# Kernel tuning notes

Hardware: AMD Instinct MI355X
Metric: run time of the kernel (lower is better)

The kernel has to match this reference:

```python
import jax, jax.numpy as jnp
import numpy as np

EPS_BN = 1e-5
EPS_NORM = 1e-12
NUM_HEADS = 8


def _bn_relu(x):
    # BatchNorm2d in training mode with fresh params (gamma=1, beta=0), then ReLU.
    m = x.mean((0, 2, 3), keepdims=True)
    v = x.var((0, 2, 3), keepdims=True)  # biased variance, as PyTorch uses for normalization
    return jax.nn.relu((x - m) * jax.lax.rsqrt(v + EPS_BN))


def _conv3(x, w, groups=1):
    # 3x3 conv, stride 1, padding 1 (NCHW / OIHW)
    return jax.lax.conv_general_dilated(
        x, w, (1, 1), ((1, 1), (1, 1)),
        dimension_numbers=('NCHW', 'OIHW', 'NCHW'),
        feature_group_count=groups)


def _encoder(x, w1, w2, w3):
    # Conv1x1 -> BN -> ReLU -> Conv k2 s2 -> BN -> ReLU -> Conv1x1 -> BN -> ReLU
    x = _bn_relu(jnp.einsum('bihw,oi->bohw', x, w1))
    b, c, h, w = x.shape
    # k=2,s=2 conv as a reshape + einsum (non-overlapping 2x2 patches)
    x = _bn_relu(jnp.einsum('bchpwq,ocpq->bohw', x.reshape(b, c, h // 2, 2, w // 2, 2), w2))
    return _bn_relu(jnp.einsum('bihw,oi->bohw', x, w3))


def _decoder(x, w1, w2, w3):
    # ConvT1x1 -> BN -> ReLU -> ConvT k2 s2 -> BN -> ReLU -> ConvT1x1 -> BN -> ReLU
    x = _bn_relu(jnp.einsum('bihw,io->bohw', x, w1))
    # ConvTranspose k=2,s=2: each input pixel expands to a 2x2 block
    y = jnp.einsum('bihw,iopq->bohpwq', x, w2)
    b, o, h, p, w, q = y.shape
    x = _bn_relu(y.reshape(b, o, h * p, w * q))
    return _bn_relu(jnp.einsum('bihw,io->bohw', x, w3))


def _l2norm(x):
    # F.normalize(dim=-1) with eps=1e-12
    return x / jnp.maximum(jnp.linalg.norm(x, axis=-1, keepdims=True), EPS_NORM)


def setup_inputs() -> dict:
    key = jax.random.key(0)
    ks = jax.random.split(key, 13)
    B, C, H, W = 8, 256, 64, 64
    d = C // 4  # attention dim after self.divide

    def rn(k, shape, s=0.1):
        return jax.random.normal(k, shape, jnp.float32) * s

    return {
        'x': jax.random.normal(ks[0], (B, C, H, W), jnp.float32),
        'y': jax.random.normal(ks[1], (B, C, H, W), jnp.float32),
        'temperature': jnp.ones((NUM_HEADS, 1, 1), jnp.float32),
        'enc_w1': rn(ks[2], (d // 2, C)),
        'enc_w2': rn(ks[3], (d // 2, d // 2, 2, 2)),
        'enc_w3': rn(ks[4], (d, d // 2)),
        'kv_w': rn(ks[5], (2 * d, d)),
        'kv_dw_w': rn(ks[6], (2 * d, 1, 3, 3)),
        'q_w': rn(ks[7], (d, d)),
        'q_dw_w': rn(ks[8], (d, d, 3, 3)),
        'proj_w': rn(ks[9], (d, d)),
        'dec_w1': rn(ks[10], (d, 2 * d)),
        'dec_w2': rn(ks[11], (2 * d, 2 * d, 2, 2)),
        'dec_w3': rn(ks[12], (2 * d, 4 * d)),
    }


def reference(x, y, temperature, enc_w1, enc_w2, enc_w3, kv_w, kv_dw_w,
              q_w, q_dw_w, proj_w, dec_w1, dec_w2, dec_w3):
    # Shared freshly-built encoder applied to both x and y (same weights,
    # BN batch stats computed per call).
    x = _encoder(x, enc_w1, enc_w2, enc_w3)
    y = _encoder(y, enc_w1, enc_w2, enc_w3)
    b, c, h, w = x.shape  # c = 64, h = w = 32

    kv = _conv3(jnp.einsum('bihw,oi->bohw', x, kv_w), kv_dw_w, groups=2 * c)
    k, v = jnp.split(kv, 2, axis=1)
    q = _conv3(jnp.einsum('bihw,oi->bohw', y, q_w), q_dw_w)  # regular 3x3 conv

    ch = c // NUM_HEADS
    heads = lambda t: t.reshape(b, NUM_HEADS, ch, h * w)  # b head c (h w)
    q, k, v = heads(q), heads(k), heads(v)
    q = _l2norm(q)
    k = _l2norm(k)
    temp = temperature[None]  # [1, head, 1, 1]

    # Spatial attention: [b, head, hw, hw]
    attn_s = jax.nn.softmax(jnp.einsum('bhcn,bhcm->bhnm', q, k) * temp, axis=-1)
    out_s = jnp.einsum('bhcn,bhnm->bhcm', v, attn_s).reshape(b, c, h, w)
    out_s = jnp.einsum('bihw,oi->bohw', out_s, proj_w)

    # Channel attention: [b, head, c, c]
    attn_c = jax.nn.softmax(jnp.einsum('bhcn,bhdn->bhcd', q, k) * temp, axis=-1)
    out_c = jnp.einsum('bhcd,bhdn->bhcn', attn_c, v).reshape(b, c, h, w)
    out_c = jnp.einsum('bihw,oi->bohw', out_c, proj_w)

    return _decoder(out_s + out_c, dec_w1, dec_w2, dec_w3)
```

## Files before the change

### kernel.cpp

```cpp
#include <hip/hip_runtime.h>
#include <hip/hip_bf16.h>

#define EPS_BN 1e-5f

template<int OT, bool HASBN, bool HASSTATS>
__global__ __launch_bounds__(256) void conv1x1_kernel(
    const float* __restrict__ in0, const float* __restrict__ in1,
    const float* __restrict__ w, float* __restrict__ out,
    const float* __restrict__ stIn, float* __restrict__ stOut,
    int I, int O, int P, int wio, int zsplit, float invN)
{
  __shared__ float wl[2048];
  __shared__ float bnm[256], bnr[256];
  int tid = threadIdx.x;
  int o0 = blockIdx.y*OT;
  int z  = blockIdx.z;
  int t  = (z >= zsplit) ? 1 : 0;
  int b  = t ? (z - zsplit) : z;
  const float* in = t ? in1 : in0;

  for(int idx=tid; idx<I*OT; idx+=256){
    int i = idx/OT, j = idx - i*OT;
    wl[idx] = wio ? w[(size_t)i*O + o0 + j] : w[(size_t)(o0+j)*I + i];
  }
  if(HASBN){
    for(int i=tid; i<I; i+=256){
      float s  = stIn[((size_t)t*I + i)*2];
      float s2 = stIn[((size_t)t*I + i)*2+1];
      float m  = s*invN;
      bnm[i] = m;
      bnr[i] = rsqrtf(s2*invN - m*m + EPS_BN);
    }
  }
  __syncthreads();

  int p4 = blockIdx.x*256 + tid;
  const float4* inb = (const float4*)(in + (size_t)b*I*P) + p4;
  int P4 = P >> 2;

  float acc[OT][4];
#pragma unroll
  for(int j=0;j<OT;j++){ acc[j][0]=acc[j][1]=acc[j][2]=acc[j][3]=0.f; }

  float4 vb[8];
  for(int i0=0;i0<I;i0+=8){
#pragma unroll
    for(int u=0;u<8;u++) vb[u] = inb[(size_t)(i0+u)*P4];
#pragma unroll
    for(int u=0;u<8;u++){
      float4 v = vb[u];
      if(HASBN){
        float m = bnm[i0+u], r = bnr[i0+u];
        v.x = fmaxf((v.x-m)*r, 0.f); v.y = fmaxf((v.y-m)*r, 0.f);
        v.z = fmaxf((v.z-m)*r, 0.f); v.w = fmaxf((v.w-m)*r, 0.f);
      }
      const float* wr = &wl[(i0+u)*OT];
#pragma unroll
      for(int j=0;j<OT;j++){
        float wv = wr[j];
        acc[j][0] = fmaf(wv, v.x, acc[j][0]);
        acc[j][1] = fmaf(wv, v.y, acc[j][1]);
        acc[j][2] = fmaf(wv, v.z, acc[j][2]);
        acc[j][3] = fmaf(wv, v.w, acc[j][3]);
      }
    }
  }

  float4* ob = (float4*)(out + ((size_t)z*O + o0)*P) + p4;
#pragma unroll
  for(int j=0;j<OT;j++){
    float4 vv = {acc[j][0], acc[j][1], acc[j][2], acc[j][3]};
    ob[(size_t)j*P4] = vv;
  }

  if(HASSTATS){
#pragma unroll
    for(int j=0;j<OT;j++){
      float s  = acc[j][0]+acc[j][1]+acc[j][2]+acc[j][3];
      float s2 = acc[j][0]*acc[j][0]+acc[j][1]*acc[j][1]
               + acc[j][2]*acc[j][2]+acc[j][3]*acc[j][3];
      for(int off=32; off>0; off>>=1){
        s  += __shfl_down(s,  off, 64);
        s2 += __shfl_down(s2, off, 64);
      }
      if((tid & 63)==0){
        atomicAdd(&stOut[((size_t)t*O + o0 + j)*2],   s);
        atomicAdd(&stOut[((size_t)t*O + o0 + j)*2+1], s2);
      }
    }
  }
}

__global__ __launch_bounds__(256) void conv2x2s2_bn_kernel(
    const float* __restrict__ in, const float* __restrict__ w,
    float* __restrict__ out, const float* __restrict__ stIn,
    float* __restrict__ stOut, float invN)
{
  __shared__ float wl[512];
  __shared__ float bnm[32], bnr[32];
  int tid = threadIdx.x;
  int o0 = blockIdx.x*4;
  int z  = blockIdx.y;
  int t  = (z >= 8) ? 1 : 0;

  for(int idx=tid; idx<512; idx+=256){
    int pq = idx & 3, r = idx >> 2;
    int i = r >> 2, j = r & 3;
    wl[idx] = w[(((size_t)(o0+j)*32 + i)*4) + pq];
  }
  if(tid < 32){
    float s  = stIn[((size_t)t*32 + tid)*2];
    float s2 = stIn[((size_t)t*32 + tid)*2+1];
    float m  = s*invN;
    bnm[tid] = m;
    bnr[tid] = rsqrtf(s2*invN - m*m + EPS_BN);
  }
  __syncthreads();

  int h  = tid >> 3;
  int wg = tid & 7;
  int cb = wg*8;

  float acc[4][4];
#pragma unroll
  for(int j=0;j<4;j++) for(int k=0;k<4;k++) acc[j][k]=0.f;

  float4 pre[8];
  for(int i0=0;i0<32;i0+=4){
#pragma unroll
    for(int u=0;u<4;u++){
      pre[2*u]   = *(const float4*)(in + (((size_t)z*32+i0+u)*64 + 2*h)*64 + cb);
      pre[2*u+1] = *(const float4*)(in + (((size_t)z*32+i0+u)*64 + 2*h)*64 + cb + 4);
    }
#pragma unroll
    for(int u=0;u<4;u++){
      int i = i0+u;
      const float4* r1p = (const float4*)(in + (((size_t)z*32+i)*64 + 2*h+1)*64 + cb);
      float4 a0 = pre[2*u], a1 = pre[2*u+1];
      float4 b0 = r1p[0], b1 = r1p[1];
      float m = bnm[i], r = bnr[i];
      float t0[8] = {a0.x,a0.y,a0.z,a0.w,a1.x,a1.y,a1.z,a1.w};
      float t1[8] = {b0.x,b0.y,b0.z,b0.w,b1.x,b1.y,b1.z,b1.w};
#pragma unroll
      for(int e=0;e<8;e++){
        t0[e] = fmaxf((t0[e]-m)*r, 0.f);
        t1[e] = fmaxf((t1[e]-m)*r, 0.f);
      }
#pragma unroll
      for(int j=0;j<4;j++){
        const float* wj = &wl[(i*4+j)*4];
#pragma unroll
        for(int k=0;k<4;k++){
          acc[j][k] = fmaf(wj[0], t0[2*k],   acc[j][k]);
          acc[j][k] = fmaf(wj[1], t0[2*k+1], acc[j][k]);
          acc[j][k] = fmaf(wj[2], t1[2*k],   acc[j][k]);
          acc[j][k] = fmaf(wj[3], t1[2*k+1], acc[j][k]);
        }
      }
    }
  }

#pragma unroll
  for(int j=0;j<4;j++){
    float4 vv = {acc[j][0],acc[j][1],acc[j][2],acc[j][3]};
    *(float4*)(out + ((size_t)z*32 + o0+j)*1024 + h*32 + wg*4) = vv;
  }
#pragma unroll
  for(int j=0;j<4;j++){
    float s  = acc[j][0]+acc[j][1]+acc[j][2]+acc[j][3];
    float s2 = acc[j][0]*acc[j][0]+acc[j][1]*acc[j][1]
             + acc[j][2]*acc[j][2]+acc[j][3]*acc[j][3];
    for(int off=32; off>0; off>>=1){
      s  += __shfl_down(s,  off, 64);
      s2 += __shfl_down(s2, off, 64);
    }
    if((tid & 63)==0){
      atomicAdd(&stOut[((size_t)t*32 + o0 + j)*2],   s);
      atomicAdd(&stOut[((size_t)t*32 + o0 + j)*2+1], s2);
    }
  }
}

__global__ __launch_bounds__(256) void upsample2x2_bn_kernel(
    const float* __restrict__ in, const float* __restrict__ w,
    float* __restrict__ out, const float* __restrict__ stIn,
    float* __restrict__ stOut, float invN)
{
  __shared__ float wl[1024];
  __shared__ float bnm[128], bnr[128];
  int tid = threadIdx.x;
  int o0 = blockIdx.x*2;
  int b  = blockIdx.y;

  for(int idx=tid; idx<1024; idx+=256){
    int pq = idx & 3, r = idx >> 2;
    int i = r >> 1, j = r & 1;
    wl[idx] = w[((size_t)i*128 + o0+j)*4 + pq];
  }
  if(tid < 128){
    float s  = stIn[(size_t)tid*2];
    float s2 = stIn[(size_t)tid*2+1];
    float m  = s*invN;
    bnm[tid] = m;
    bnr[tid] = rsqrtf(s2*invN - m*m + EPS_BN);
  }
  __syncthreads();

  int h  = tid >> 3;
  int wg = tid & 7;
  int w0 = wg*4;

  float acc[2][16];
#pragma unroll
  for(int j=0;j<2;j++) for(int e=0;e<16;e++) acc[j][e]=0.f;

  float4 vb4[8];
  for(int i0=0;i0<128;i0+=8){
#pragma unroll
    for(int u=0;u<8;u++)
      vb4[u] = *(const float4*)(in + (((size_t)b*128+i0+u)*1024) + h*32 + w0);
#pragma unroll
    for(int u=0;u<8;u++){
      int i = i0+u;
      float4 v = vb4[u];
      float m = bnm[i], r = bnr[i];
      float vk[4] = {fmaxf((v.x-m)*r,0.f), fmaxf((v.y-m)*r,0.f),
                     fmaxf((v.z-m)*r,0.f), fmaxf((v.w-m)*r,0.f)};
#pragma unroll
      for(int j=0;j<2;j++){
        const float* wj = &wl[(i*2+j)*4];
#pragma unroll
        for(int pq=0;pq<4;pq++){
#pragma unroll
          for(int k=0;k<4;k++)
            acc[j][pq*4+k] = fmaf(wj[pq], vk[k], acc[j][pq*4+k]);
        }
      }
    }
  }

#pragma unroll
  for(int j=0;j<2;j++){
    float* ob = out + ((size_t)b*128 + o0+j)*4096;
#pragma unroll
    for(int p=0;p<2;p++){
      float4 A = {acc[j][(p*2+0)*4+0], acc[j][(p*2+1)*4+0],
                  acc[j][(p*2+0)*4+1], acc[j][(p*2+1)*4+1]};
      float4 B = {acc[j][(p*2+0)*4+2], acc[j][(p*2+1)*4+2],
                  acc[j][(p*2+0)*4+3], acc[j][(p*2+1)*4+3]};
      *(float4*)(ob + (2*h+p)*64 + 2*w0)     = A;
      *(float4*)(ob + (2*h+p)*64 + 2*w0 + 4) = B;
    }
  }

#pragma unroll
  for(int j=0;j<2;j++){
    float s=0.f, s2=0.f;
#pragma unroll
    for(int e=0;e<16;e++){ s += acc[j][e]; s2 += acc[j][e]*acc[j][e]; }
    for(int off=32; off>0; off>>=1){
      s  += __shfl_down(s,  off, 64);
      s2 += __shfl_down(s2, off, 64);
    }
    if((tid & 63)==0){
      atomicAdd(&stOut[((size_t)(o0+j))*2],   s);
      atomicAdd(&stOut[((size_t)(o0+j))*2+1], s2);
    }
  }
}

__global__ __launch_bounds__(256) void bn_final_kernel(
    float* __restrict__ x, const float* __restrict__ st, float invN)
{
  int idx4 = blockIdx.x*256 + threadIdx.x;
  int c = (idx4 >> 10) & 255;
  float s  = st[(size_t)c*2];
  float s2 = st[(size_t)c*2+1];
  float m  = s*invN;
  float r  = rsqrtf(s2*invN - m*m + EPS_BN);
  float4 v = ((float4*)x)[idx4];
  v.x = fmaxf((v.x-m)*r, 0.f); v.y = fmaxf((v.y-m)*r, 0.f);
  v.z = fmaxf((v.z-m)*r, 0.f); v.w = fmaxf((v.w-m)*r, 0.f);
  ((float4*)x)[idx4] = v;
}

__global__ __launch_bounds__(256) void dwconv3x3_kernel(
    const float* __restrict__ in, const float* __restrict__ w,
    float* __restrict__ out, int C, int H, int Wd)
{
  int idx = blockIdx.x*256 + threadIdx.x;
  int c = blockIdx.y, b = blockIdx.z;
  if(idx >= H*Wd) return;
  int h = idx / Wd, x = idx - h*Wd;
  const float* inp = in + ((size_t)b*C + c)*H*Wd;
  float acc = 0.f;
#pragma unroll
  for(int p=0;p<3;p++){
    int hh = h + p - 1;
    if((unsigned)hh >= (unsigned)H) continue;
#pragma unroll
    for(int q=0;q<3;q++){
      int wv = x + q - 1;
      if((unsigned)wv >= (unsigned)Wd) continue;
      acc += w[c*9 + p*3 + q] * inp[hh*Wd + wv];
    }
  }
  out[((size_t)b*C + c)*H*Wd + idx] = acc;
}

__global__ __launch_bounds__(256) void conv3x3_kernel(
    const float* __restrict__ in, const float* __restrict__ w,
    float* __restrict__ out, int IC, int H, int Wd)
{
  int o = blockIdx.y, b = blockIdx.z;
  __shared__ float wl[576];
  for(int t=threadIdx.x; t<IC*9; t+=256) wl[t] = w[(size_t)o*IC*9 + t];
  __syncthreads();
  int idx = blockIdx.x*256 + threadIdx.x;
  if(idx >= H*Wd) return;
  int h = idx / Wd, x = idx - h*Wd;
  const float* inb = in + (size_t)b*IC*H*Wd;
  float acc = 0.f;
  for(int i=0;i<IC;i++){
    const float* inp = inb + (size_t)i*H*Wd;
    const float* wp  = wl + i*9;
#pragma unroll
    for(int p=0;p<3;p++){
      int hh = h + p - 1;
      if((unsigned)hh >= (unsigned)H) continue;
      const float* row = inp + hh*Wd;
#pragma unroll
      for(int q=0;q<3;q++){
        int wv = x + q - 1;
        if((unsigned)wv >= (unsigned)Wd) continue;
        acc = fmaf(wp[p*3+q], row[wv], acc);
      }
    }
  }
  out[((size_t)b*gridDim.y + o)*H*Wd + idx] = acc;
}

__global__ __launch_bounds__(256) void l2norm_kernel(
    float* __restrict__ q, float* __restrict__ kv)
{
  int r = blockIdx.x;
  float* p;
  if(r < 512){ int b=r>>6, c=r&63; p = q + ((size_t)b*64+c)*1024; }
  else { int rr=r-512; int b=rr>>6, c=rr&63; p = kv + ((size_t)b*128+c)*1024; }
  int tid = threadIdx.x;
  float4 v = ((float4*)p)[tid];
  float s = v.x*v.x + v.y*v.y + v.z*v.z + v.w*v.w;
  __shared__ float ls[256];
  ls[tid]=s; __syncthreads();
  for(int st=128; st>0; st>>=1){ if(tid<st) ls[tid]+=ls[tid+st]; __syncthreads(); }
  float scale = 1.f / fmaxf(sqrtf(ls[0]), 1e-12f);
  v.x*=scale; v.y*=scale; v.z*=scale; v.w*=scale;
  ((float4*)p)[tid] = v;
}

__global__ __launch_bounds__(256) void attn_pass1(
    const float* __restrict__ q, const float* __restrict__ kv,
    const float* __restrict__ temp, float* __restrict__ iden_out)
{
  int chunk = blockIdx.x, hh = blockIdx.y, b = blockIdx.z;
  int tid = threadIdx.x;
  __shared__ __align__(16) float kl[8192];
  const float* kb = kv + ((size_t)b*128 + hh*8)*1024;
  for(int t=tid;t<8192;t+=256){ int c=t>>10, m=t&1023; kl[m*8+c]=kb[t]; }
  __syncthreads();
  int n = chunk*256 + tid;
  const float* qp = q + ((size_t)b*64 + hh*8)*1024 + n;
  float qr[8];
#pragma unroll
  for(int c=0;c<8;c++) qr[c]=qp[(size_t)c*1024];
  float th = temp[hh];
  float mxb = fabsf(th);
  const float4* kl4 = (const float4*)kl;
  float den = 0.f;
  for(int m=0;m<1024;m++){
    float4 a = kl4[2*m], a2 = kl4[2*m+1];
    float s = qr[0]*a.x+qr[1]*a.y+qr[2]*a.z+qr[3]*a.w
            + qr[4]*a2.x+qr[5]*a2.y+qr[6]*a2.z+qr[7]*a2.w;
    den += __expf(s*th - mxb);
  }
  int bh = b*8+hh;
  iden_out[(size_t)bh*1024+n] = 1.f/den;
}

__global__ __launch_bounds__(256) void attn_pass2(
    const float* __restrict__ q, const float* __restrict__ kv,
    const float* __restrict__ temp, const float* __restrict__ iden_in,
    float* __restrict__ out)
{
  int chunk = blockIdx.x, hh = blockIdx.y, b = blockIdx.z;
  int tid = threadIdx.x;
  __shared__ __align__(16) float ql[4096];
  __shared__ __align__(16) float vl[4096];
  const float* qb = q  + ((size_t)b*64 + hh*8)*1024;
  const float* vb = kv + ((size_t)b*128 + 64 + hh*8)*1024;
  int bh = b*8+hh;
  int m = chunk*256 + tid;
  const float* kb = kv + ((size_t)b*128 + hh*8)*1024 + m;
  float kr[8];
#pragma unroll
  for(int c=0;c<8;c++) kr[c]=kb[(size_t)c*1024];
  float th = temp[hh];
  float mxb = fabsf(th);
  const float* idp = iden_in + (size_t)bh*1024;
  float acc[8] = {0,0,0,0,0,0,0,0};
  for(int half=0; half<2; half++){
    int n0 = half*512;
    __syncthreads();
    for(int t=tid; t<4096; t+=256){
      int c = t>>9, n = t&511;
      ql[n*8+c] = qb[(size_t)c*1024 + n0 + n];
      vl[n*8+c] = vb[(size_t)c*1024 + n0 + n];
    }
    __syncthreads();
    const float4* ql4 = (const float4*)ql;
    const float4* vl4 = (const float4*)vl;
    for(int n=0;n<512;n++){
      float4 qa = ql4[2*n], qa2 = ql4[2*n+1];
      float s = kr[0]*qa.x+kr[1]*qa.y+kr[2]*qa.z+kr[3]*qa.w
              + kr[4]*qa2.x+kr[5]*qa2.y+kr[6]*qa2.z+kr[7]*qa2.w;
      float pp = __expf(s*th - mxb) * idp[n0+n];
      float4 va = vl4[2*n], va2 = vl4[2*n+1];
      acc[0]+=pp*va.x; acc[1]+=pp*va.y; acc[2]+=pp*va.z; acc[3]+=pp*va.w;
      acc[4]+=pp*va2.x; acc[5]+=pp*va2.y; acc[6]+=pp*va2.z; acc[7]+=pp*va2.w;
    }
  }
  float* ob = out + ((size_t)b*64 + hh*8)*1024 + m;
#pragma unroll
  for(int c=0;c<8;c++) ob[(size_t)c*1024] = acc[c];
}

__global__ __launch_bounds__(256) void attn_channel(
    const float* __restrict__ q, const float* __restrict__ kv,
    const float* __restrict__ temp, float* out)
{
  int hh = blockIdx.x, b = blockIdx.y;
  __shared__ float kl[8192];
  const float* qb = q  + ((size_t)b*64 + hh*8)*1024;
  const float* kb = kv + ((size_t)b*128 + hh*8)*1024;
  const float* vb = kv + ((size_t)b*128 + 64 + hh*8)*1024;
  int tid = threadIdx.x;
  for(int t=tid;t<8192;t+=256) kl[t]=kb[t];
  __syncthreads();
  __shared__ float part[256];
  __shared__ float a[64];
  {
    int pair = tid >> 2, seg = tid & 3;
    int c = pair >> 3, d = pair & 7;
    const float* qrow = qb + (size_t)c*1024 + seg*256;
    const float* krow = kl + d*1024 + seg*256;
    float s = 0.f;
#pragma unroll 4
    for(int n=0;n<256;n++) s += qrow[n]*krow[n];
    part[tid] = s;
  }
  __syncthreads();
  if(tid < 64){
    float g = part[tid*4]+part[tid*4+1]+part[tid*4+2]+part[tid*4+3];
    part[tid] = g * temp[hh];
  }
  __syncthreads();
  if(tid < 8){
    float mx = -3.4e38f;
    for(int d=0;d<8;d++) mx = fmaxf(mx, part[tid*8+d]);
    float den = 0.f;
    float e[8];
    for(int d=0;d<8;d++){ e[d] = __expf(part[tid*8+d]-mx); den+=e[d]; }
    float inv = 1.f/den;
    for(int d=0;d<8;d++) a[tid*8+d] = e[d]*inv;
  }
  __syncthreads();
  float* ob = out + ((size_t)b*64 + hh*8)*1024;
  for(int n=tid;n<1024;n+=256){
    float vv[8];
#pragma unroll
    for(int d=0;d<8;d++) vv[d] = vb[(size_t)d*1024+n];
#pragma unroll
    for(int c=0;c<8;c++){
      float s = 0.f;
#pragma unroll
      for(int d=0;d<8;d++) s += a[c*8+d]*vv[d];
      ob[(size_t)c*1024+n] += s;
    }
  }
}

extern "C" void kernel_launch(void* const* d_in, const int* in_sizes, int n_in,
                              void* d_out, int out_size, void* d_ws, size_t ws_size,
                              hipStream_t stream)
{
  (void)in_sizes; (void)n_in; (void)out_size; (void)ws_size;
  const float* x      = (const float*)d_in[0];
  const float* y      = (const float*)d_in[1];
  const float* temp   = (const float*)d_in[2];
  const float* enc_w1 = (const float*)d_in[3];
  const float* enc_w2 = (const float*)d_in[4];
  const float* enc_w3 = (const float*)d_in[5];
  const float* kv_w   = (const float*)d_in[6];
  const float* kv_dw_w= (const float*)d_in[7];
  const float* q_w    = (const float*)d_in[8];
  const float* q_dw_w = (const float*)d_in[9];
  const float* proj_w = (const float*)d_in[10];
  const float* dec_w1 = (const float*)d_in[11];
  const float* dec_w2 = (const float*)d_in[12];
  const float* dec_w3 = (const float*)d_in[13];
  float* out = (float*)d_out;

  float* W   = (float*)d_ws;
  float* ST  = W;
  float* ST0 = ST;
  float* ST1 = ST + 128;
  float* ST2 = ST + 256;
  float* ST3 = ST + 512;
  float* ST4 = ST + 768;
  float* ST5 = ST + 1024;
  float* A    = W + 2048;
  float* E1   = A;
  float* KV1  = A;
  float* QPre = A + 1048576;
  float* ATTN = A;
  float* PROJ = A + 524288;
  float* D1   = A + 1048576;
  float* E2   = W + 2099200;
  float* E3   = W + 2623488;
  float* KV   = W + 3672064;
  float* Q    = W + 4720640;
  float* IDEN = W + 5244928;
  float* D2   = W + 2099200;

  const float inv32k = 1.f/32768.f, inv8k = 1.f/8192.f;

  hipMemsetAsync(ST, 0, 2048*sizeof(float), stream);

  conv1x1_kernel<4,false,true><<<dim3(4,8,16),256,0,stream>>>(
      x, y, enc_w1, E1, nullptr, ST0, 256, 32, 4096, 0, 8, 0.f);
  conv2x2s2_bn_kernel<<<dim3(8,16),256,0,stream>>>(E1, enc_w2, E2, ST0, ST1, inv32k);
  conv1x1_kernel<2,true,true><<<dim3(1,32,16),256,0,stream>>>(
      E2, E2 + (size_t)8*32*1024, enc_w3, E3, ST1, ST2, 32, 64, 1024, 0, 8, inv8k);

  conv1x1_kernel<4,true,false><<<dim3(1,32,8),256,0,stream>>>(
      E3, E3, kv_w, KV1, ST2, nullptr, 64, 128, 1024, 0, 999, inv8k);
  dwconv3x3_kernel<<<dim3(4,128,8),256,0,stream>>>(KV1, kv_dw_w, KV, 128, 32, 32);
  conv1x1_kernel<2,true,false><<<dim3(1,32,8),256,0,stream>>>(
      E3 + (size_t)8*64*1024, E3, q_w, QPre, ST2 + 128, nullptr, 64, 64, 1024, 0, 999, inv8k);
  conv3x3_kernel<<<dim3(4,64,8),256,0,stream>>>(QPre, q_dw_w, Q, 64, 32, 32);

  l2norm_kernel<<<1024,256,0,stream>>>(Q, KV);

  attn_pass1<<<dim3(4,8,8),256,0,stream>>>(Q, KV, temp, IDEN);
  attn_pass2<<<dim3(4,8,8),256,0,stream>>>(Q, KV, temp, IDEN, ATTN);
  attn_channel<<<dim3(8,8),256,0,stream>>>(Q, KV, temp, ATTN);

  conv1x1_kernel<2,false,false><<<dim3(1,32,8),256,0,stream>>>(
      ATTN, ATTN, proj_w, PROJ, nullptr, nullptr, 64, 64, 1024, 0, 999, 0.f);

  conv1x1_kernel<4,false,true><<<dim3(1,32,8),256,0,stream>>>(
      PROJ, PROJ, dec_w1, D1, nullptr, ST3, 64, 128, 1024, 1, 999, 0.f);
  upsample2x2_bn_kernel<<<dim3(64,8),256,0,stream>>>(D1, dec_w2, D2, ST3, ST4, inv8k);
  conv1x1_kernel<8,true,true><<<dim3(4,32,8),256,0,stream>>>(
      D2, D2, dec_w3, out, ST4, ST5, 128, 256, 4096, 1, 999, inv32k);
  bn_final_kernel<<<8192,256,0,stream>>>(out, ST5, inv32k);
}
```

Baseline: 678.1 us.

## Split attention passes across key halves with atomics, add tiled encoder conv

Adds a register-tiled first encoder 1x1 conv kernel that computes 4x4 output blocks per thread from shared-memory tiles, with wave-shuffle stat reduction. Both spatial attention passes are split into two halves over the reduction dimension, doubling the block count. Partial results are combined through atomicAdd into buffers zeroed beforehand by memset. The passes also use padded shared-memory strides, pre-scale q and k by temperature, and unroll by two. Two 1x1 convs get smaller output tiles and more blocks, trading extra atomics and memsets for more parallelism on a small grid.

```diff
diff --git a/kernel.cpp b/kernel.cpp
--- a/kernel.cpp
+++ b/kernel.cpp
@@ -2,6 +2,78 @@
 #include <hip/hip_bf16.h>
 
 #define EPS_BN 1e-5f
+
+__global__ __launch_bounds__(256) void conv1x1_enc1_kernel(
+    const float* __restrict__ in0, const float* __restrict__ in1,
+    const float* __restrict__ w, float* __restrict__ out,
+    float* __restrict__ stOut)
+{
+  __shared__ float il[32*128];
+  __shared__ float wt[32*32];
+  int tid  = threadIdx.x;
+  int tile = blockIdx.x;
+  int z    = blockIdx.y;
+  int t    = z >> 3;
+  const float* in  = t ? in1 : in0;
+  const float* inb = in + ((size_t)(z&7))*256*4096 + tile*128;
+  int cg = tid & 31;
+  int og = tid >> 5;
+
+  float acc[4][4];
+#pragma unroll
+  for(int j=0;j<4;j++){ acc[j][0]=acc[j][1]=acc[j][2]=acc[j][3]=0.f; }
+
+  for(int k0=0; k0<256; k0+=32){
+    __syncthreads();
+#pragma unroll
+    for(int u=0;u<4;u++){
+      int fid = tid + u*256;
+      int ch = fid >> 5, c4 = fid & 31;
+      ((float4*)il)[fid] = *(const float4*)(inb + (size_t)(k0+ch)*4096 + c4*4);
+    }
+#pragma unroll
+    for(int u=0;u<4;u++){
+      int idx = tid + u*256;
+      int o = idx >> 5, ch = idx & 31;
+      wt[ch*32 + o] = w[(size_t)o*256 + k0 + ch];
+    }
+    __syncthreads();
+#pragma unroll 8
+    for(int ch=0; ch<32; ch++){
+      float4 v  = ((float4*)il)[ch*32 + cg];
+      float4 wv = ((float4*)wt)[ch*8 + og];
+      acc[0][0]=fmaf(wv.x,v.x,acc[0][0]); acc[0][1]=fmaf(wv.x,v.y,acc[0][1]);
+      acc[0][2]=fmaf(wv.x,v.z,acc[0][2]); acc[0][3]=fmaf(wv.x,v.w,acc[0][3]);
+      acc[1][0]=fmaf(wv.y,v.x,acc[1][0]); acc[1][1]=fmaf(wv.y,v.y,acc[1][1]);
+      acc[1][2]=fmaf(wv.y,v.z,acc[1][2]); acc[1][3]=fmaf(wv.y,v.w,acc[1][3]);
+      acc[2][0]=fmaf(wv.z,v.x,acc[2][0]); acc[2][1]=fmaf(wv.z,v.y,acc[2][1]);
+      acc[2][2]=fmaf(wv.z,v.z,acc[2][2]); acc[2][3]=fmaf(wv.z,v.w,acc[2][3]);
+      acc[3][0]=fmaf(wv.w,v.x,acc[3][0]); acc[3][1]=fmaf(wv.w,v.y,acc[3][1]);
+      acc[3][2]=fmaf(wv.w,v.z,acc[3][2]); acc[3][3]=fmaf(wv.w,v.w,acc[3][3]);
+    }
+  }
+
+  float* ob = out + ((size_t)z*32 + og*4)*4096 + tile*128 + cg*4;
+#pragma unroll
+  for(int j=0;j<4;j++){
+    float4 vv = {acc[j][0],acc[j][1],acc[j][2],acc[j][3]};
+    *(float4*)(ob + (size_t)j*4096) = vv;
+  }
+#pragma unroll
+  for(int j=0;j<4;j++){
+    float s  = acc[j][0]+acc[j][1]+acc[j][2]+acc[j][3];
+    float s2 = acc[j][0]*acc[j][0]+acc[j][1]*acc[j][1]
+             + acc[j][2]*acc[j][2]+acc[j][3]*acc[j][3];
+    for(int off=16; off>0; off>>=1){
+      s  += __shfl_down(s,  off, 64);
+      s2 += __shfl_down(s2, off, 64);
+    }
+    if((tid & 31)==0){
+      atomicAdd(&stOut[((size_t)t*32 + og*4 + j)*2],   s);
+      atomicAdd(&stOut[((size_t)t*32 + og*4 + j)*2+1], s2);
+    }
+  }
+}
 
 template<int OT, bool HASBN, bool HASSTATS>
 __global__ __launch_bounds__(256) void conv1x1_kernel(
@@ -360,78 +432,88 @@
 
 __global__ __launch_bounds__(256) void attn_pass1(
     const float* __restrict__ q, const float* __restrict__ kv,
-    const float* __restrict__ temp, float* __restrict__ iden_out)
-{
-  int chunk = blockIdx.x, hh = blockIdx.y, b = blockIdx.z;
+    const float* __restrict__ temp, float* __restrict__ den_out)
+{
+  int bx = blockIdx.x, hh = blockIdx.y, b = blockIdx.z;
+  int nchunk = bx >> 1, mh = bx & 1;
   int tid = threadIdx.x;
-  __shared__ __align__(16) float kl[8192];
-  const float* kb = kv + ((size_t)b*128 + hh*8)*1024;
-  for(int t=tid;t<8192;t+=256){ int c=t>>10, m=t&1023; kl[m*8+c]=kb[t]; }
-  __syncthreads();
-  int n = chunk*256 + tid;
+  __shared__ __align__(16) float kl[512*12];
+  const float* kb = kv + ((size_t)b*128 + hh*8)*1024 + mh*512;
+  for(int t=tid;t<4096;t+=256){ int c=t>>9, m=t&511; kl[m*12+c]=kb[(size_t)c*1024+m]; }
+  __syncthreads();
+  int n = nchunk*256 + tid;
   const float* qp = q + ((size_t)b*64 + hh*8)*1024 + n;
-  float qr[8];
-#pragma unroll
-  for(int c=0;c<8;c++) qr[c]=qp[(size_t)c*1024];
   float th = temp[hh];
   float mxb = fabsf(th);
+  float qr[8];
+#pragma unroll
+  for(int c=0;c<8;c++) qr[c]=qp[(size_t)c*1024]*th;
   const float4* kl4 = (const float4*)kl;
-  float den = 0.f;
-  for(int m=0;m<1024;m++){
-    float4 a = kl4[2*m], a2 = kl4[2*m+1];
-    float s = qr[0]*a.x+qr[1]*a.y+qr[2]*a.z+qr[3]*a.w
-            + qr[4]*a2.x+qr[5]*a2.y+qr[6]*a2.z+qr[7]*a2.w;
-    den += __expf(s*th - mxb);
-  }
-  int bh = b*8+hh;
-  iden_out[(size_t)bh*1024+n] = 1.f/den;
+  float den = 0.f, den2 = 0.f;
+  for(int m=0;m<512;m+=2){
+    float4 a  = kl4[m*3],     a2 = kl4[m*3+1];
+    float4 bt = kl4[(m+1)*3], b2 = kl4[(m+1)*3+1];
+    float s0 = qr[0]*a.x+qr[1]*a.y+qr[2]*a.z+qr[3]*a.w
+             + qr[4]*a2.x+qr[5]*a2.y+qr[6]*a2.z+qr[7]*a2.w;
+    float s1 = qr[0]*bt.x+qr[1]*bt.y+qr[2]*bt.z+qr[3]*bt.w
+             + qr[4]*b2.x+qr[5]*b2.y+qr[6]*b2.z+qr[7]*b2.w;
+    den  += __expf(s0 - mxb);
+    den2 += __expf(s1 - mxb);
+  }
+  atomicAdd(&den_out[((size_t)(b*8+hh))*1024+n], den+den2);
 }
 
 __global__ __launch_bounds__(256) void attn_pass2(
     const float* __restrict__ q, const float* __restrict__ kv,
-    const float* __restrict__ temp, const float* __restrict__ iden_in,
+    const float* __restrict__ temp, const float* __restrict__ den,
     float* __restrict__ out)
 {
-  int chunk = blockIdx.x, hh = blockIdx.y, b = blockIdx.z;
+  int bx = blockIdx.x, hh = blockIdx.y, b = blockIdx.z;
+  int mchunk = bx >> 1, nh = bx & 1;
   int tid = threadIdx.x;
-  __shared__ __align__(16) float ql[4096];
-  __shared__ __align__(16) float vl[4096];
-  const float* qb = q  + ((size_t)b*64 + hh*8)*1024;
-  const float* vb = kv + ((size_t)b*128 + 64 + hh*8)*1024;
+  __shared__ __align__(16) float ql[512*12];
+  __shared__ __align__(16) float vl[512*12];
+  __shared__ float idl[512];
   int bh = b*8+hh;
-  int m = chunk*256 + tid;
+  int n0 = nh*512;
+  const float* qb = q  + ((size_t)b*64 + hh*8)*1024 + n0;
+  const float* vb = kv + ((size_t)b*128 + 64 + hh*8)*1024 + n0;
+  for(int t=tid;t<4096;t+=256){
+    int c=t>>9, n=t&511;
+    ql[n*12+c] = qb[(size_t)c*1024+n];
+    vl[n*12+c] = vb[(size_t)c*1024+n];
+  }
+  for(int u=tid;u<512;u+=256) idl[u] = 1.f/den[(size_t)bh*1024 + n0 + u];
+  __syncthreads();
+  int m = mchunk*256 + tid;
   const float* kb = kv + ((size_t)b*128 + hh*8)*1024 + m;
-  float kr[8];
-#pragma unroll
-  for(int c=0;c<8;c++) kr[c]=kb[(size_t)c*1024];
   float th = temp[hh];
   float mxb = fabsf(th);
-  const float* idp = iden_in + (size_t)bh*1024;
+  float kr[8];
+#pragma unroll
+  for(int c=0;c<8;c++) kr[c]=kb[(size_t)c*1024]*th;
   float acc[8] = {0,0,0,0,0,0,0,0};
-  for(int half=0; half<2; half++){
-    int n0 = half*512;
-    __syncthreads();
-    for(int t=tid; t<4096; t+=256){
-      int c = t>>9, n = t&511;
-      ql[n*8+c] = qb[(size_t)c*1024 + n0 + n];
-      vl[n*8+c] = vb[(size_t)c*1024 + n0 + n];
-    }
-    __syncthreads();
-    const float4* ql4 = (const float4*)ql;
-    const float4* vl4 = (const float4*)vl;
-    for(int n=0;n<512;n++){
-      float4 qa = ql4[2*n], qa2 = ql4[2*n+1];
-      float s = kr[0]*qa.x+kr[1]*qa.y+kr[2]*qa.z+kr[3]*qa.w
-              + kr[4]*qa2.x+kr[5]*qa2.y+kr[6]*qa2.z+kr[7]*qa2.w;
-      float pp = __expf(s*th - mxb) * idp[n0+n];
-      float4 va = vl4[2*n], va2 = vl4[2*n+1];
-      acc[0]+=pp*va.x; acc[1]+=pp*va.y; acc[2]+=pp*va.z; acc[3]+=pp*va.w;
-      acc[4]+=pp*va2.x; acc[5]+=pp*va2.y; acc[6]+=pp*va2.z; acc[7]+=pp*va2.w;
-    }
+  const float4* ql4 = (const float4*)ql;
+  const float4* vl4 = (const float4*)vl;
+  for(int n=0;n<512;n+=2){
+    float4 qa = ql4[n*3],     qa2 = ql4[n*3+1];
+    float4 qb4= ql4[(n+1)*3], qb2 = ql4[(n+1)*3+1];
+    float s0 = kr[0]*qa.x+kr[1]*qa.y+kr[2]*qa.z+kr[3]*qa.w
+             + kr[4]*qa2.x+kr[5]*qa2.y+kr[6]*qa2.z+kr[7]*qa2.w;
+    float s1 = kr[0]*qb4.x+kr[1]*qb4.y+kr[2]*qb4.z+kr[3]*qb4.w
+             + kr[4]*qb2.x+kr[5]*qb2.y+kr[6]*qb2.z+kr[7]*qb2.w;
+    float p0 = __expf(s0 - mxb) * idl[n];
+    float p1 = __expf(s1 - mxb) * idl[n+1];
+    float4 va = vl4[n*3],     va2 = vl4[n*3+1];
+    float4 vb4f= vl4[(n+1)*3], vb2 = vl4[(n+1)*3+1];
+    acc[0]+=p0*va.x + p1*vb4f.x; acc[1]+=p0*va.y + p1*vb4f.y;
+    acc[2]+=p0*va.z + p1*vb4f.z; acc[3]+=p0*va.w + p1*vb4f.w;
+    acc[4]+=p0*va2.x + p1*vb2.x; acc[5]+=p0*va2.y + p1*vb2.y;
+    acc[6]+=p0*va2.z + p1*vb2.z; acc[7]+=p0*va2.w + p1*vb2.w;
   }
   float* ob = out + ((size_t)b*64 + hh*8)*1024 + m;
 #pragma unroll
-  for(int c=0;c<8;c++) ob[(size_t)c*1024] = acc[c];
+  for(int c=0;c<8;c++) atomicAdd(&ob[(size_t)c*1024], acc[c]);
 }
 
 __global__ __launch_bounds__(256) void attn_channel(
@@ -529,36 +611,38 @@
   float* E3   = W + 2623488;
   float* KV   = W + 3672064;
   float* Q    = W + 4720640;
-  float* IDEN = W + 5244928;
+  float* DEN  = W + 5244928;
   float* D2   = W + 2099200;
 
   const float inv32k = 1.f/32768.f, inv8k = 1.f/8192.f;
 
   hipMemsetAsync(ST, 0, 2048*sizeof(float), stream);
-
-  conv1x1_kernel<4,false,true><<<dim3(4,8,16),256,0,stream>>>(
-      x, y, enc_w1, E1, nullptr, ST0, 256, 32, 4096, 0, 8, 0.f);
+  hipMemsetAsync(DEN, 0, 65536*sizeof(float), stream);
+
+  conv1x1_enc1_kernel<<<dim3(32,16),256,0,stream>>>(x, y, enc_w1, E1, ST0);
   conv2x2s2_bn_kernel<<<dim3(8,16),256,0,stream>>>(E1, enc_w2, E2, ST0, ST1, inv32k);
   conv1x1_kernel<2,true,true><<<dim3(1,32,16),256,0,stream>>>(
       E2, E2 + (size_t)8*32*1024, enc_w3, E3, ST1, ST2, 32, 64, 1024, 0, 8, inv8k);
 
-  conv1x1_kernel<4,true,false><<<dim3(1,32,8),256,0,stream>>>(
+  conv1x1_kernel<2,true,false><<<dim3(1,64,8),256,0,stream>>>(
       E3, E3, kv_w, KV1, ST2, nullptr, 64, 128, 1024, 0, 999, inv8k);
   dwconv3x3_kernel<<<dim3(4,128,8),256,0,stream>>>(KV1, kv_dw_w, KV, 128, 32, 32);
   conv1x1_kernel<2,true,false><<<dim3(1,32,8),256,0,stream>>>(
       E3 + (size_t)8*64*1024, E3, q_w, QPre, ST2 + 128, nullptr, 64, 64, 1024, 0, 999, inv8k);
   conv3x3_kernel<<<dim3(4,64,8),256,0,stream>>>(QPre, q_dw_w, Q, 64, 32, 32);
 
+  hipMemsetAsync(ATTN, 0, 524288*sizeof(float), stream);
+
   l2norm_kernel<<<1024,256,0,stream>>>(Q, KV);
 
-  attn_pass1<<<dim3(4,8,8),256,0,stream>>>(Q, KV, temp, IDEN);
-  attn_pass2<<<dim3(4,8,8),256,0,stream>>>(Q, KV, temp, IDEN, ATTN);
+  attn_pass1<<<dim3(8,8,8),256,0,stream>>>(Q, KV, temp, DEN);
+  attn_pass2<<<dim3(8,8,8),256,0,stream>>>(Q, KV, temp, DEN, ATTN);
   attn_channel<<<dim3(8,8),256,0,stream>>>(Q, KV, temp, ATTN);
 
   conv1x1_kernel<2,false,false><<<dim3(1,32,8),256,0,stream>>>(
       ATTN, ATTN, proj_w, PROJ, nullptr, nullptr, 64, 64, 1024, 0, 999, 0.f);
 
-  conv1x1_kernel<4,false,true><<<dim3(1,32,8),256,0,stream>>>(
+  conv1x1_kernel<2,false,true><<<dim3(1,64,8),256,0,stream>>>(
       PROJ, PROJ, dec_w1, D1, nullptr, ST3, 64, 128, 1024, 1, 999, 0.f);
   upsample2x2_bn_kernel<<<dim3(64,8),256,0,stream>>>(D1, dec_w2, D2, ST3, ST4, inv8k);
   conv1x1_kernel<8,true,true><<<dim3(4,32,8),256,0,stream>>>(
```

Result: faster. 637.5 us (-6.0%).
